# Performance work log

Measured on AMD Instinct MI355X. Metric: run time of the kernel, lower is better.

Reference implementation:

```python
import jax, jax.numpy as jnp
import numpy as np

B, D_IN, H, L, K, E, NL = 16384, 768, 1024, 128, 8192, 128, 3
CC = 0.25  # commitment cost
sg = jax.lax.stop_gradient


def _ln(x, g, b):
    # torch nn.LayerNorm, eps=1e-5
    m = jnp.mean(x, -1, keepdims=True)
    v = jnp.mean((x - m) ** 2, -1, keepdims=True)
    return (x - m) / jnp.sqrt(v + 1e-5) * g + b


def setup_inputs() -> dict:
    key = jax.random.key(0)
    ks = iter(jax.random.split(key, 32))
    def n(sh, s=0.02):
        return jax.random.normal(next(ks), sh, jnp.float32) * s
    return dict(
        x=jax.random.normal(next(ks), (B, D_IN), jnp.float32),
        eps=jax.random.normal(next(ks), (B, L), jnp.float32),
        enc_w1=n((D_IN, H)), enc_b1=jnp.zeros((H,), jnp.float32),
        enc_w2=n((H, H)), enc_b2=jnp.zeros((H,), jnp.float32),
        enc_w3=n((H, H)), enc_b3=jnp.zeros((H,), jnp.float32),
        mu_w=n((H, L)), mu_b=jnp.zeros((L,), jnp.float32),
        var_w=n((H, L)), var_b=jnp.zeros((L,), jnp.float32),
        dec_w1=n((L, H)), dec_b1=jnp.zeros((H,), jnp.float32),
        dec_w2=n((H, H)), dec_b2=jnp.zeros((H,), jnp.float32),
        dec_w3=n((H, D_IN)), dec_b3=jnp.zeros((D_IN,), jnp.float32),
        ln_g=jnp.ones((NL, L), jnp.float32),
        ln_b=jnp.zeros((NL, L), jnp.float32),
        q_in_w=n((NL, L, E)), q_in_b=jnp.zeros((NL, E), jnp.float32),
        codebook=jax.random.uniform(next(ks), (NL, K, E), jnp.float32,
                                    -1.0 / K, 1.0 / K),
        q_out_w=n((NL, E, L)), q_out_b=jnp.zeros((NL, L), jnp.float32),
    )


def reference(x, eps, enc_w1, enc_b1, enc_w2, enc_b2, enc_w3, enc_b3,
              mu_w, mu_b, var_w, var_b,
              dec_w1, dec_b1, dec_w2, dec_b2, dec_w3, dec_b3,
              ln_g, ln_b, q_in_w, q_in_b, codebook, q_out_w, q_out_b):
    # encoder MLP
    h = jax.nn.relu(x @ enc_w1 + enc_b1)
    h = jax.nn.relu(h @ enc_w2 + enc_b2)
    h = h @ enc_w3 + enc_b3
    mu = h @ mu_w + mu_b
    log_var = h @ var_w + var_b
    z = mu + eps * jnp.exp(0.5 * log_var)  # reparameterize

    # residual quantization over NL layers
    cur = z
    quantized = jnp.zeros_like(z)
    total_loss = jnp.float32(0.0)
    for i in range(NL):  # small fixed layer count
        nr = _ln(cur, ln_g[i], ln_b[i])                  # [B, L]
        f = nr @ q_in_w[i] + q_in_b[i]                   # [B, E]
        cb = codebook[i]                                 # [K, E]
        d = (jnp.sum(f * f, axis=1, keepdims=True)
             + jnp.sum(cb * cb, axis=1)
             - 2.0 * f @ cb.T)                           # [B, K]
        idx = jnp.argmin(d, axis=1)                      # [B]
        q = cb[idx] @ q_out_w[i] + q_out_b[i]            # gather == onehot@cb
        e_loss = jnp.mean((sg(q) - nr) ** 2)
        q_loss = jnp.mean((q - sg(nr)) ** 2)
        total_loss = total_loss + q_loss + CC * e_loss
        q_st = nr + sg(q - nr)                           # straight-through
        quantized = quantized + q_st
        cur = cur - q_st

    # decoder MLP
    r = jax.nn.relu(quantized @ dec_w1 + dec_b1)
    r = jax.nn.relu(r @ dec_w2 + dec_b2)
    recon = r @ dec_w3 + dec_b3
    return recon, mu, log_var, total_loss
```

## Files before the change

kernel.cpp:

```cpp
#include <hip/hip_runtime.h>
#include <stdint.h>


typedef float   floatx4  __attribute__((ext_vector_type(4)));
typedef __bf16  bf16x8   __attribute__((ext_vector_type(8)));
typedef unsigned short ushort4v __attribute__((ext_vector_type(4)));
typedef unsigned short bfbits;

#define AS1 __attribute__((address_space(1)))
#define AS3 __attribute__((address_space(3)))

__device__ __forceinline__ bfbits f2bf(float f) {
  unsigned u = __float_as_uint(f);
  u += 0x7fffu + ((u >> 16) & 1u);
  return (bfbits)(u >> 16);
}

__device__ __forceinline__ void load_lds16(const void* g, void* l) {
  __builtin_amdgcn_global_load_lds((AS1 void*)g, (AS3 void*)l, 16, 0, 0);
}

__global__ __launch_bounds__(256) void cvt_bf16_kernel(
    const float* __restrict__ in, bfbits* __restrict__ out, long n4) {
  long i = (long)blockIdx.x * 256 + threadIdx.x;
  if (i >= n4) return;
  float4 v = ((const float4*)in)[i];
  ushort4v o = { f2bf(v.x), f2bf(v.y), f2bf(v.z), f2bf(v.w) };
  ((ushort4v*)out)[i] = o;
}

__global__ __launch_bounds__(256) void transpose_bf16_kernel(
    const float* __restrict__ W, bfbits* __restrict__ Wt, int K, int N) {
  __shared__ float t[32][33];
  const long base = (long)blockIdx.z * K * N;
  const int k0 = blockIdx.y * 32, n0 = blockIdx.x * 32;
  const int tx = threadIdx.x & 31, ty = threadIdx.x >> 5;
#pragma unroll
  for (int j = 0; j < 32; j += 8)
    t[ty + j][tx] = W[base + (long)(k0 + ty + j) * N + n0 + tx];
  __syncthreads();
#pragma unroll
  for (int j = 0; j < 32; j += 8)
    Wt[base + (long)(n0 + ty + j) * K + k0 + tx] = f2bf(t[tx][ty + j]);
}

__global__ __launch_bounds__(256) void rownorm_kernel(
    const float* __restrict__ cb, float* __restrict__ out) {
  const int wave = threadIdx.x >> 6, lane = threadIdx.x & 63;
  const long row = (long)blockIdx.x * 4 + wave;
  const float* r = cb + row * 128;
  float a = r[lane], b = r[lane + 64];
  float s = a * a + b * b;
#pragma unroll
  for (int off = 1; off < 64; off <<= 1) s += __shfl_xor(s, off);
  if (lane == 0) out[row] = s;
}

template <bool RELU, bool OUTF32, bool DUAL>
__global__ __launch_bounds__(256) void gemm_kernel(
    const bfbits* __restrict__ A, const bfbits* __restrict__ Bt,
    const float* __restrict__ bias, bfbits* __restrict__ Cb,
    float* __restrict__ Cf, float* __restrict__ Cf2, int N, int Kd) {
  __shared__ bfbits Als[128 * 64];
  __shared__ bfbits Bls[128 * 64];
  const int tid = threadIdx.x;
  const int wave = tid >> 6, lane = tid & 63;
  const int wr = wave >> 1, wc = wave & 1;
  const int row0 = blockIdx.x << 7, col0 = blockIdx.y << 7;
  const int l15 = lane & 15, l16 = lane >> 4;
  const int jrow = lane >> 3;
  const int gchunk = (lane & 7) ^ jrow;

  floatx4 acc[4][4] = {};

  for (int k0 = 0; k0 < Kd; k0 += 64) {
    __syncthreads();
#pragma unroll
    for (int j = 0; j < 4; ++j) {
      const int gi = wave * 4 + j;
      const int r = gi * 8 + jrow;
      load_lds16(A + (long)(row0 + r) * Kd + (k0 + gchunk * 8),
                 Als + gi * 512 + lane * 8);
      load_lds16(Bt + (long)(col0 + r) * Kd + (k0 + gchunk * 8),
                 Bls + gi * 512 + lane * 8);
    }
    __syncthreads();
#pragma unroll
    for (int kk = 0; kk < 2; ++kk) {
      bf16x8 af[4], bf[4];
#pragma unroll
      for (int t = 0; t < 4; ++t) {
        const int ar = wr * 64 + t * 16 + l15;
        af[t] = *(const bf16x8*)(Als + ar * 64 + (((kk * 4 + l16) ^ (ar & 7)) * 8));
        const int br = wc * 64 + t * 16 + l15;
        bf[t] = *(const bf16x8*)(Bls + br * 64 + (((kk * 4 + l16) ^ (br & 7)) * 8));
      }
#pragma unroll
      for (int i = 0; i < 4; ++i)
#pragma unroll
        for (int jn = 0; jn < 4; ++jn)
          acc[i][jn] = __builtin_amdgcn_mfma_f32_16x16x32_bf16(
              af[i], bf[jn], acc[i][jn], 0, 0, 0);
    }
  }

#pragma unroll
  for (int mt = 0; mt < 4; ++mt) {
#pragma unroll
    for (int nt = 0; nt < 4; ++nt) {
      const int col = col0 + wc * 64 + nt * 16 + l15;
      const float bv = bias[col];
      const int rowb = row0 + wr * 64 + mt * 16 + l16 * 4;
#pragma unroll
      for (int r = 0; r < 4; ++r) {
        float v = acc[mt][nt][r] + bv;
        if (RELU) v = fmaxf(v, 0.f);
        if (DUAL) {
          if (col < 128) Cf[(long)(rowb + r) * 128 + col] = v;
          else           Cf2[(long)(rowb + r) * 128 + col - 128] = v;
        } else {
          const long idx = (long)(rowb + r) * N + col;
          if (OUTF32) Cf[idx] = v; else Cb[idx] = f2bf(v);
        }
      }
    }
  }
}

template <bool RELU, bool OUTF32>
__global__ __launch_bounds__(512, 2) void gemm256_kernel(
    const bfbits* __restrict__ A, const bfbits* __restrict__ Bt,
    const float* __restrict__ bias, bfbits* __restrict__ Cb,
    float* __restrict__ Cf, int N, int Kd) {
  __shared__ alignas(16) bfbits As[2][256 * 64];
  __shared__ alignas(16) bfbits Bs[2][256 * 64];
  const int tid = threadIdx.x;
  const int w = tid >> 6, lane = tid & 63;
  const int wr = w >> 2, wc = w & 3;
  const int l15 = lane & 15, l16 = lane >> 4;
  const int jrow = lane >> 3;
  const int gch = (lane & 7) ^ jrow;

  const int nbx = gridDim.x, nby = gridDim.y;
  const int nwg = nbx * nby;
  const int cpx = nwg >> 3;
  const int lid = blockIdx.y * nbx + blockIdx.x;
  const int swz = (lid & 7) * cpx + (lid >> 3);
  const int bm = swz / nby, bn = swz % nby;
  const long row0 = (long)bm << 8;
  const long col0 = (long)bn << 8;

  const int NT = Kd >> 6;

  auto stageA = [&](int t, int hh) {
    const bfbits* src = A + (row0 + hh * 128) * Kd + t * 64 + gch * 8;
    bfbits* dst = &As[t & 1][hh * 8192];
#pragma unroll
    for (int q = 0; q < 2; ++q) {
      const int gi = q * 8 + w;
      load_lds16(src + (long)(gi * 8 + jrow) * Kd, dst + gi * 512 + lane * 8);
    }
  };
  auto stageB = [&](int t, int hh) {
    const bfbits* src = Bt + (col0 + hh * 128) * Kd + t * 64 + gch * 8;
    bfbits* dst = &Bs[t & 1][hh * 8192];
#pragma unroll
    for (int q = 0; q < 2; ++q) {
      const int gi = q * 8 + w;
      load_lds16(src + (long)(gi * 8 + jrow) * Kd, dst + gi * 512 + lane * 8);
    }
  };

  auto rdA = [&](int p, int i, int kk) -> bf16x8 {
    const int r = wr * 128 + i * 16 + l15;
    return *(const bf16x8*)(&As[p][r * 64 + (((kk * 4 + l16) ^ (r & 7)) * 8)]);
  };
  auto rdB = [&](int p, int j, int kk) -> bf16x8 {
    const int r = wc * 64 + j * 16 + l15;
    return *(const bf16x8*)(&Bs[p][r * 64 + (((kk * 4 + l16) ^ (r & 7)) * 8)]);
  };

  floatx4 acc[8][4] = {};

  stageA(0, 0); stageA(0, 1); stageB(0, 0); stageB(0, 1);
  stageA(1, 0);
  asm volatile("s_waitcnt vmcnt(2)" ::: "memory");
  __builtin_amdgcn_s_barrier();

  for (int s = 0; s < NT; ++s) {
    const int p = s & 1;
    bf16x8 bfr[4];

    {
      bf16x8 af[4];
#pragma unroll
      for (int t = 0; t < 4; ++t) af[t] = rdA(p, t, 0);
#pragma unroll
      for (int t = 0; t < 4; ++t) bfr[t] = rdB(p, t, 0);
      if (s + 1 < NT) stageA(s + 1, 1);
      __builtin_amdgcn_s_barrier();
      asm volatile("s_waitcnt lgkmcnt(0)" ::: "memory");
      __builtin_amdgcn_sched_barrier(0);
      __builtin_amdgcn_s_setprio(1);
#pragma unroll
      for (int i = 0; i < 4; ++i)
#pragma unroll
        for (int j = 0; j < 4; ++j)
          acc[i][j] = __builtin_amdgcn_mfma_f32_16x16x32_bf16(
              af[i], bfr[j], acc[i][j], 0, 0, 0);
      __builtin_amdgcn_s_setprio(0);
      __builtin_amdgcn_s_barrier();
    }
    {
      bf16x8 af[4];
#pragma unroll
      for (int t = 0; t < 4; ++t) af[t] = rdA(p, 4 + t, 0);
      if (s + 1 < NT) stageB(s + 1, 0);
      __builtin_amdgcn_s_barrier();
      asm volatile("s_waitcnt lgkmcnt(0)" ::: "memory");
      __builtin_amdgcn_sched_barrier(0);
      __builtin_amdgcn_s_setprio(1);
#pragma unroll
      for (int i = 0; i < 4; ++i)
#pragma unroll
        for (int j = 0; j < 4; ++j)
          acc[4 + i][j] = __builtin_amdgcn_mfma_f32_16x16x32_bf16(
              af[i], bfr[j], acc[4 + i][j], 0, 0, 0);
      __builtin_amdgcn_s_setprio(0);
      __builtin_amdgcn_s_barrier();
    }
    {
      bf16x8 af[4];
#pragma unroll
      for (int t = 0; t < 4; ++t) af[t] = rdA(p, t, 1);
#pragma unroll
      for (int t = 0; t < 4; ++t) bfr[t] = rdB(p, t, 1);
      if (s + 1 < NT) stageB(s + 1, 1);
      __builtin_amdgcn_s_barrier();
      asm volatile("s_waitcnt lgkmcnt(0)" ::: "memory");
      __builtin_amdgcn_sched_barrier(0);
      __builtin_amdgcn_s_setprio(1);
#pragma unroll
      for (int i = 0; i < 4; ++i)
#pragma unroll
        for (int j = 0; j < 4; ++j)
          acc[i][j] = __builtin_amdgcn_mfma_f32_16x16x32_bf16(
              af[i], bfr[j], acc[i][j], 0, 0, 0);
      __builtin_amdgcn_s_setprio(0);
      __builtin_amdgcn_s_barrier();
    }
    {
      bf16x8 af[4];
#pragma unroll
      for (int t = 0; t < 4; ++t) af[t] = rdA(p, 4 + t, 1);
      __builtin_amdgcn_s_barrier();
      asm volatile("s_waitcnt lgkmcnt(0)" ::: "memory");
      __builtin_amdgcn_sched_barrier(0);
      __builtin_amdgcn_s_setprio(1);
#pragma unroll
      for (int i = 0; i < 4; ++i)
#pragma unroll
        for (int j = 0; j < 4; ++j)
          acc[4 + i][j] = __builtin_amdgcn_mfma_f32_16x16x32_bf16(
              af[i], bfr[j], acc[4 + i][j], 0, 0, 0);
      __builtin_amdgcn_s_setprio(0);
      __builtin_amdgcn_s_barrier();
    }
    if (s + 1 < NT) {
      if (s + 2 < NT) {
        stageA(s + 2, 0);
        asm volatile("s_waitcnt vmcnt(2)" ::: "memory");
      } else {
        asm volatile("s_waitcnt vmcnt(0)" ::: "memory");
      }
      __builtin_amdgcn_s_barrier();
    }
  }

#pragma unroll
  for (int i = 0; i < 8; ++i) {
    const long rowb = row0 + wr * 128 + i * 16 + l16 * 4;
#pragma unroll
    for (int j = 0; j < 4; ++j) {
      const int col = (int)col0 + wc * 64 + j * 16 + l15;
      const float bv = bias[col];
#pragma unroll
      for (int r = 0; r < 4; ++r) {
        float v = acc[i][j][r] + bv;
        if (RELU) v = fmaxf(v, 0.f);
        const long idx = (rowb + r) * N + col;
        if (OUTF32) Cf[idx] = v; else Cb[idx] = f2bf(v);
      }
    }
  }
}

template <bool OUTF32>
__global__ __launch_bounds__(256) void gemm_n128_kernel(
    const bfbits* __restrict__ A, const bfbits* __restrict__ Bt,
    const float* __restrict__ bias, bfbits* __restrict__ Cb,
    float* __restrict__ Cf) {
  __shared__ bfbits Als[64 * 64];
  __shared__ bfbits Bls[128 * 64];
  const int tid = threadIdx.x;
  const int wave = tid >> 6, lane = tid & 63;
  const int wr = wave >> 1, wc = wave & 1;
  const int row0 = blockIdx.x << 6;
  const int l15 = lane & 15, l16 = lane >> 4;
  const int jrow = lane >> 3;
  const int gchunk = (lane & 7) ^ jrow;

  floatx4 acc[2][4] = {};

  for (int k0 = 0; k0 < 128; k0 += 64) {
    __syncthreads();
    {
#pragma unroll
      for (int j = 0; j < 2; ++j) {
        const int gi = wave * 2 + j;
        const int r = gi * 8 + jrow;
        load_lds16(A + (long)(row0 + r) * 128 + (k0 + gchunk * 8),
                   Als + gi * 512 + lane * 8);
      }
#pragma unroll
      for (int j = 0; j < 4; ++j) {
        const int gi = wave * 4 + j;
        const int r = gi * 8 + jrow;
        load_lds16(Bt + (long)r * 128 + (k0 + gchunk * 8),
                   Bls + gi * 512 + lane * 8);
      }
    }
    __syncthreads();
#pragma unroll
    for (int kk = 0; kk < 2; ++kk) {
      bf16x8 af[2], bf[4];
#pragma unroll
      for (int t = 0; t < 2; ++t) {
        const int ar = wr * 32 + t * 16 + l15;
        af[t] = *(const bf16x8*)(Als + ar * 64 + (((kk * 4 + l16) ^ (ar & 7)) * 8));
      }
#pragma unroll
      for (int t = 0; t < 4; ++t) {
        const int br = wc * 64 + t * 16 + l15;
        bf[t] = *(const bf16x8*)(Bls + br * 64 + (((kk * 4 + l16) ^ (br & 7)) * 8));
      }
#pragma unroll
      for (int i = 0; i < 2; ++i)
#pragma unroll
        for (int jn = 0; jn < 4; ++jn)
          acc[i][jn] = __builtin_amdgcn_mfma_f32_16x16x32_bf16(
              af[i], bf[jn], acc[i][jn], 0, 0, 0);
    }
  }

#pragma unroll
  for (int mt = 0; mt < 2; ++mt) {
#pragma unroll
    for (int nt = 0; nt < 4; ++nt) {
      const int col = wc * 64 + nt * 16 + l15;
      const float bv = bias[col];
      const int rowb = row0 + wr * 32 + mt * 16 + l16 * 4;
#pragma unroll
      for (int r = 0; r < 4; ++r) {
        const float v = acc[mt][nt][r] + bv;
        const long idx = (long)(rowb + r) * 128 + col;
        if (OUTF32) Cf[idx] = v; else Cb[idx] = f2bf(v);
      }
    }
  }
}

__global__ __launch_bounds__(512, 2) void dist2_kernel(
    const bfbits* __restrict__ A,
    const bfbits* __restrict__ Bt,
    const float* __restrict__ cbnorm,
    int2* __restrict__ cand) {
  __shared__ alignas(16) bfbits Bls[2][128 * 128];
  const int tid = threadIdx.x;
  const int wave = tid >> 6, lane = tid & 63;
  const int wr = wave & 3, wc = wave >> 2;
  const int l15 = lane & 15, l16 = lane >> 4;
  const int row0 = blockIdx.y * 256;
  const int col0 = blockIdx.x * 2048;

  bf16x8 af[4][4];
#pragma unroll
  for (int mt = 0; mt < 4; ++mt)
#pragma unroll
    for (int s = 0; s < 4; ++s)
      af[mt][s] = *(const bf16x8*)(A + (long)(row0 + wr * 64 + mt * 16 + l15) * 128 +
                                   s * 32 + l16 * 8);

  auto stage = [&](int t, int p) {
    const bfbits* src = Bt + (long)(col0 + t * 128) * 128;
    bfbits* dst = &Bls[p][0];
#pragma unroll
    for (int q = 0; q < 4; ++q) {
      const int j = q * 512 + tid;
      const int c = j >> 4;
      const int g = (j & 15) ^ (c & 15);
      load_lds16(src + (long)c * 128 + g * 8, dst + (size_t)j * 8);
    }
  };

  stage(0, 0);

  float run_val[4][4];
  int   run_col[4][4];
#pragma unroll
  for (int mt = 0; mt < 4; ++mt)
#pragma unroll
    for (int r = 0; r < 4; ++r) { run_val[mt][r] = 3.0e38f; run_col[mt][r] = 0; }

  __syncthreads();

  for (int t = 0; t < 16; ++t) {
    const bfbits* buf = &Bls[t & 1][0];
    if (t + 1 < 16) stage(t + 1, (t + 1) & 1);

    float cn[4];
    int   colv[4];
#pragma unroll
    for (int nt = 0; nt < 4; ++nt) {
      const int cl = wc * 64 + nt * 16 + l15;
      cn[nt] = cbnorm[col0 + t * 128 + cl];
      colv[nt] = t * 128 + cl;
    }

    floatx4 acc[4][4] = {};
#pragma unroll
    for (int s = 0; s < 4; ++s) {
      bf16x8 bf[4];
#pragma unroll
      for (int nt = 0; nt < 4; ++nt) {
        const int cl = wc * 64 + nt * 16 + l15;
        bf[nt] = *(const bf16x8*)(buf + (size_t)cl * 128 +
                                  (size_t)(((s * 4 + l16) ^ l15)) * 8);
      }
#pragma unroll
      for (int mt = 0; mt < 4; ++mt)
#pragma unroll
        for (int nt = 0; nt < 4; ++nt)
          acc[mt][nt] = __builtin_amdgcn_mfma_f32_16x16x32_bf16(
              af[mt][s], bf[nt], acc[mt][nt], 0, 0, 0);
    }

#pragma unroll
    for (int mt = 0; mt < 4; ++mt)
#pragma unroll
      for (int nt = 0; nt < 4; ++nt)
#pragma unroll
        for (int r = 0; r < 4; ++r) {
          const float sc = fmaf(-2.0f, acc[mt][nt][r], cn[nt]);
          if (sc < run_val[mt][r]) { run_val[mt][r] = sc; run_col[mt][r] = colv[nt]; }
        }

    __syncthreads();
  }

#pragma unroll
  for (int mt = 0; mt < 4; ++mt)
#pragma unroll
    for (int r = 0; r < 4; ++r) {
      float v = run_val[mt][r];
      int   c = run_col[mt][r];
#pragma unroll
      for (int off = 1; off < 16; off <<= 1) {
        const float ov = __shfl_xor(v, off);
        const int   oc = __shfl_xor(c, off);
        if (ov < v || (ov == v && oc < c)) { v = ov; c = oc; }
      }
      if (l15 == 0) {
        const int row = row0 + wr * 64 + mt * 16 + l16 * 4 + r;
        cand[(long)row * 8 + blockIdx.x * 2 + wc] =
            make_int2(__float_as_int(v), col0 + c);
      }
    }
}

__global__ __launch_bounds__(256) void argmin8_kernel(
    const int2* __restrict__ cand, const float* __restrict__ cb,
    bfbits* __restrict__ cbg) {
  const int wave = threadIdx.x >> 6, lane = threadIdx.x & 63;
  const long row = (long)blockIdx.x * 4 + wave;
  float v = 3.0e38f; int k = 0x7fffffff;
  if (lane < 8) {
    int2 c = cand[row * 8 + lane];
    v = __int_as_float(c.x); k = c.y;
  }
#pragma unroll
  for (int off = 1; off < 8; off <<= 1) {
    float ov = __shfl_xor(v, off);
    int   ok = __shfl_xor(k, off);
    if (ov < v || (ov == v && ok < k)) { v = ov; k = ok; }
  }
  k = __shfl(k, 0);
  const float* src = cb + (long)k * 128;
  cbg[row * 128 + lane]      = f2bf(src[lane]);
  cbg[row * 128 + lane + 64] = f2bf(src[lane + 64]);
}

__device__ __forceinline__ void ln_row(float c0, float c1, int lane,
                                       const float* __restrict__ g,
                                       const float* __restrict__ bta,
                                       long row, bfbits* __restrict__ nrb,
                                       float* __restrict__ nrf) {
  float s = c0 + c1, sq = c0 * c0 + c1 * c1;
#pragma unroll
  for (int off = 1; off < 64; off <<= 1) {
    s += __shfl_xor(s, off);
    sq += __shfl_xor(sq, off);
  }
  const float m = s * (1.f / 128.f);
  const float var = fmaxf(sq * (1.f / 128.f) - m * m, 0.f);
  const float rstd = rsqrtf(var + 1e-5f);
  const float y0 = (c0 - m) * rstd * g[lane] + bta[lane];
  const float y1 = (c1 - m) * rstd * g[lane + 64] + bta[lane + 64];
  nrf[row * 128 + lane] = y0;
  nrf[row * 128 + lane + 64] = y1;
  nrb[row * 128 + lane] = f2bf(y0);
  nrb[row * 128 + lane + 64] = f2bf(y1);
}

__global__ __launch_bounds__(256) void reparam_ln_kernel(
    const float* __restrict__ mu, const float* __restrict__ lv,
    const float* __restrict__ eps, float* __restrict__ cur,
    float* __restrict__ qnt, const float* __restrict__ g,
    const float* __restrict__ bta, bfbits* __restrict__ nrb,
    float* __restrict__ nrf) {
  const int wave = threadIdx.x >> 6, lane = threadIdx.x & 63;
  const long row = (long)blockIdx.x * 4 + wave;
  const long i0 = row * 128 + lane, i1 = i0 + 64;
  const float z0 = mu[i0] + eps[i0] * expf(0.5f * lv[i0]);
  const float z1 = mu[i1] + eps[i1] * expf(0.5f * lv[i1]);
  cur[i0] = z0; cur[i1] = z1;
  qnt[i0] = 0.f; qnt[i1] = 0.f;
  ln_row(z0, z1, lane, g, bta, row, nrb, nrf);
}

template <bool DO_LN>
__global__ __launch_bounds__(256) void qupd_ln_kernel(
    const float* __restrict__ q, float* __restrict__ nrf,
    float* __restrict__ cur, float* __restrict__ qnt,
    const float* __restrict__ g, const float* __restrict__ bta,
    bfbits* __restrict__ nrb, float* __restrict__ lossp) {
  const int wave = threadIdx.x >> 6, lane = threadIdx.x & 63;
  const long row = (long)blockIdx.x * 4 + wave;
  const long i0 = row * 128 + lane, i1 = i0 + 64;
  const float q0 = q[i0], q1 = q[i1];
  const float d0 = q0 - nrf[i0], d1 = q1 - nrf[i1];
  qnt[i0] += q0; qnt[i1] += q1;
  float p = d0 * d0 + d1 * d1;
#pragma unroll
  for (int off = 1; off < 64; off <<= 1) p += __shfl_xor(p, off);
  __shared__ float sp[4];
  if (lane == 0) sp[wave] = p;
  __syncthreads();
  if (threadIdx.x == 0) lossp[blockIdx.x] = sp[0] + sp[1] + sp[2] + sp[3];
  if (DO_LN) {
    const float c0 = cur[i0] - q0, c1 = cur[i1] - q1;
    cur[i0] = c0; cur[i1] = c1;
    ln_row(c0, c1, lane, g, bta, row, nrb, nrf);
  }
}

__global__ __launch_bounds__(256) void loss_reduce_kernel(
    const float* __restrict__ lossp, float* __restrict__ out, int n) {
  float s = 0.f;
  for (int i = threadIdx.x; i < n; i += 256) s += lossp[i];
#pragma unroll
  for (int off = 1; off < 64; off <<= 1) s += __shfl_xor(s, off);
  __shared__ float sp[4];
  const int wave = threadIdx.x >> 6, lane = threadIdx.x & 63;
  if (lane == 0) sp[wave] = s;
  __syncthreads();
  if (threadIdx.x == 0)
    *out = (sp[0] + sp[1] + sp[2] + sp[3]) * (1.25f / 2097152.f);
}

static void launch_gemm(bool relu, bool outf32, const bfbits* A,
                        const bfbits* Bt, const float* bias, bfbits* Cb,
                        float* Cf, int M, int N, int Kd, hipStream_t s) {
  dim3 g(M / 128, N / 128), b(256);
  if (relu) {
    gemm_kernel<true, false, false><<<g, b, 0, s>>>(A, Bt, bias, Cb, Cf, nullptr, N, Kd);
  } else if (outf32) {
    gemm_kernel<false, true, false><<<g, b, 0, s>>>(A, Bt, bias, Cb, Cf, nullptr, N, Kd);
  } else {
    gemm_kernel<false, false, false><<<g, b, 0, s>>>(A, Bt, bias, Cb, Cf, nullptr, N, Kd);
  }
}

static void launch_gemm256(bool relu, bool outf32, const bfbits* A,
                           const bfbits* Bt, const float* bias, bfbits* Cb,
                           float* Cf, int M, int N, int Kd, hipStream_t s) {
  dim3 g(M / 256, N / 256), b(512);
  if (relu) {
    gemm256_kernel<true, false><<<g, b, 0, s>>>(A, Bt, bias, Cb, Cf, N, Kd);
  } else if (outf32) {
    gemm256_kernel<false, true><<<g, b, 0, s>>>(A, Bt, bias, Cb, Cf, N, Kd);
  } else {
    gemm256_kernel<false, false><<<g, b, 0, s>>>(A, Bt, bias, Cb, Cf, N, Kd);
  }
}

extern "C" void kernel_launch(void* const* d_in, const int* in_sizes, int n_in,
                              void* d_out, int out_size, void* d_ws,
                              size_t ws_size, hipStream_t stream) {
  (void)in_sizes; (void)n_in; (void)out_size; (void)ws_size;
  constexpr long B = 16384, DIN = 768, H = 1024, L = 128, K = 8192;

  const float* x    = (const float*)d_in[0];
  const float* eps  = (const float*)d_in[1];
  const float* ew1  = (const float*)d_in[2];
  const float* eb1  = (const float*)d_in[3];
  const float* ew2  = (const float*)d_in[4];
  const float* eb2  = (const float*)d_in[5];
  const float* ew3  = (const float*)d_in[6];
  const float* eb3  = (const float*)d_in[7];
  const float* muw  = (const float*)d_in[8];
  const float* mub  = (const float*)d_in[9];
  const float* vaw  = (const float*)d_in[10];
  const float* vab  = (const float*)d_in[11];
  const float* dw1  = (const float*)d_in[12];
  const float* db1  = (const float*)d_in[13];
  const float* dw2  = (const float*)d_in[14];
  const float* db2  = (const float*)d_in[15];
  const float* dw3  = (const float*)d_in[16];
  const float* db3  = (const float*)d_in[17];
  const float* lng  = (const float*)d_in[18];
  const float* lnb  = (const float*)d_in[19];
  const float* qinw = (const float*)d_in[20];
  const float* qinb = (const float*)d_in[21];
  const float* cb   = (const float*)d_in[22];
  const float* qow  = (const float*)d_in[23];
  const float* qob  = (const float*)d_in[24];

  float* out = (float*)d_out;
  float* out_mu   = out + B * DIN;
  float* out_lv   = out_mu + B * L;
  float* out_loss = out_lv + B * L;

  char* ws = (char*)d_ws;
  constexpr size_t O_W1T  = 0;
  constexpr size_t O_W2T  = O_W1T + 1024 * 768 * 2;
  constexpr size_t O_W3T  = O_W2T + 1024 * 1024 * 2;
  constexpr size_t O_MUT  = O_W3T + 1024 * 1024 * 2;
  constexpr size_t O_VART = O_MUT + 128 * 1024 * 2;
  constexpr size_t O_DW1T = O_VART + 128 * 1024 * 2;
  constexpr size_t O_DW2T = O_DW1T + 1024 * 128 * 2;
  constexpr size_t O_DW3T = O_DW2T + 1024 * 1024 * 2;
  constexpr size_t O_QINT = O_DW3T + 768 * 1024 * 2;
  constexpr size_t O_QOUT = O_QINT + 3 * 128 * 128 * 2;
  constexpr size_t O_CBB  = O_QOUT + 3 * 128 * 128 * 2;
  constexpr size_t O_CBN  = O_CBB + 3 * 8192 * 128 * 2;
  constexpr size_t O_B2   = O_CBN + 3 * 8192 * 4;
  constexpr size_t O_LOSSP= O_B2 + 256 * 4;
  constexpr size_t O_CUR  = O_LOSSP + 3 * 4096 * 4;
  constexpr size_t O_QNT  = O_CUR + B * L * 4;
  constexpr size_t O_NRF  = O_QNT + B * L * 4;
  constexpr size_t O_H1   = O_NRF + B * L * 4;
  constexpr size_t O_H2   = O_H1 + B * H * 2;
  constexpr size_t O_H3   = O_H2 + B * H * 2;
  constexpr size_t O_NRB  = O_H2;
  constexpr size_t O_FB   = O_H2 + B * L * 2;
  constexpr size_t O_CBG  = O_H2 + 2 * B * L * 2;
  constexpr size_t O_QBUF = O_H2 + 3 * B * L * 2;
  constexpr size_t O_CAND = O_H2 + 3 * B * L * 2 + B * L * 4;
  constexpr size_t O_XB   = O_H3;
  constexpr size_t O_QZB  = O_H3;

  bfbits* w1t  = (bfbits*)(ws + O_W1T);
  bfbits* w2t  = (bfbits*)(ws + O_W2T);
  bfbits* w3t  = (bfbits*)(ws + O_W3T);
  bfbits* mut  = (bfbits*)(ws + O_MUT);
  bfbits* vart = (bfbits*)(ws + O_VART);
  bfbits* dw1t = (bfbits*)(ws + O_DW1T);
  bfbits* dw2t = (bfbits*)(ws + O_DW2T);
  bfbits* dw3t = (bfbits*)(ws + O_DW3T);
  bfbits* qint = (bfbits*)(ws + O_QINT);
  bfbits* qout = (bfbits*)(ws + O_QOUT);
  bfbits* cbb  = (bfbits*)(ws + O_CBB);
  float*  cbn  = (float*)(ws + O_CBN);
  float*  bias2= (float*)(ws + O_B2);
  float*  lossp= (float*)(ws + O_LOSSP);
  float*  cur  = (float*)(ws + O_CUR);
  float*  qnt  = (float*)(ws + O_QNT);
  float*  nrf  = (float*)(ws + O_NRF);
  bfbits* h1   = (bfbits*)(ws + O_H1);
  bfbits* h2   = (bfbits*)(ws + O_H2);
  bfbits* h3   = (bfbits*)(ws + O_H3);
  bfbits* nrb  = (bfbits*)(ws + O_NRB);
  bfbits* fb   = (bfbits*)(ws + O_FB);
  bfbits* cbg  = (bfbits*)(ws + O_CBG);
  float*  qbuf = (float*)(ws + O_QBUF);
  int2*   cand = (int2*)(ws + O_CAND);
  bfbits* xb   = (bfbits*)(ws + O_XB);
  bfbits* qzb  = (bfbits*)(ws + O_QZB);
  bfbits* r1   = h1;
  bfbits* r2   = h2;

  cvt_bf16_kernel<<<dim3((B * DIN) / 4 / 256), dim3(256), 0, stream>>>(x, xb, (B * DIN) / 4);
  cvt_bf16_kernel<<<dim3((3 * K * 128) / 4 / 256), dim3(256), 0, stream>>>(cb, cbb, (3 * K * 128) / 4);
  transpose_bf16_kernel<<<dim3(1024 / 32, 768 / 32, 1), dim3(256), 0, stream>>>(ew1, w1t, 768, 1024);
  transpose_bf16_kernel<<<dim3(32, 32, 1), dim3(256), 0, stream>>>(ew2, w2t, 1024, 1024);
  transpose_bf16_kernel<<<dim3(32, 32, 1), dim3(256), 0, stream>>>(ew3, w3t, 1024, 1024);
  transpose_bf16_kernel<<<dim3(128 / 32, 32, 1), dim3(256), 0, stream>>>(muw, mut, 1024, 128);
  transpose_bf16_kernel<<<dim3(128 / 32, 32, 1), dim3(256), 0, stream>>>(vaw, vart, 1024, 128);
  transpose_bf16_kernel<<<dim3(32, 128 / 32, 1), dim3(256), 0, stream>>>(dw1, dw1t, 128, 1024);
  transpose_bf16_kernel<<<dim3(32, 32, 1), dim3(256), 0, stream>>>(dw2, dw2t, 1024, 1024);
  transpose_bf16_kernel<<<dim3(768 / 32, 32, 1), dim3(256), 0, stream>>>(dw3, dw3t, 1024, 768);
  transpose_bf16_kernel<<<dim3(4, 4, 3), dim3(256), 0, stream>>>(qinw, qint, 128, 128);
  transpose_bf16_kernel<<<dim3(4, 4, 3), dim3(256), 0, stream>>>(qow, qout, 128, 128);
  rownorm_kernel<<<dim3(3 * K / 4), dim3(256), 0, stream>>>(cb, cbn);
  hipMemcpyAsync(bias2, mub, 128 * 4, hipMemcpyDeviceToDevice, stream);
  hipMemcpyAsync(bias2 + 128, vab, 128 * 4, hipMemcpyDeviceToDevice, stream);

  launch_gemm256(true, false, xb, w1t, eb1, h1, nullptr, B, 1024, 768, stream);
  launch_gemm256(true, false, h1, w2t, eb2, h2, nullptr, B, 1024, 1024, stream);
  launch_gemm256(false, false, h2, w3t, eb3, h3, nullptr, B, 1024, 1024, stream);
  gemm_kernel<false, true, true><<<dim3(128, 2), dim3(256), 0, stream>>>(
      h3, mut, bias2, nullptr, out_mu, out_lv, 256, 1024);

  reparam_ln_kernel<<<dim3(B / 4), dim3(256), 0, stream>>>(
      out_mu, out_lv, eps, cur, qnt, lng, lnb, nrb, nrf);

  for (int i = 0; i < 3; ++i) {
    gemm_n128_kernel<false><<<dim3(B / 64), dim3(256), 0, stream>>>(
        nrb, qint + (size_t)i * 128 * 128, qinb + i * 128, fb, nullptr);
    dist2_kernel<<<dim3(4, 64), dim3(512), 0, stream>>>(
        fb, cbb + (size_t)i * K * 128, cbn + (size_t)i * K, cand);
    argmin8_kernel<<<dim3(B / 4), dim3(256), 0, stream>>>(
        cand, cb + (size_t)i * K * 128, cbg);
    gemm_n128_kernel<true><<<dim3(B / 64), dim3(256), 0, stream>>>(
        cbg, qout + (size_t)i * 128 * 128, qob + i * 128, nullptr, qbuf);
    if (i < 2) {
      qupd_ln_kernel<true><<<dim3(B / 4), dim3(256), 0, stream>>>(
          qbuf, nrf, cur, qnt, lng + (i + 1) * 128, lnb + (i + 1) * 128,
          nrb, lossp + (size_t)i * 4096);
    } else {
      qupd_ln_kernel<false><<<dim3(B / 4), dim3(256), 0, stream>>>(
          qbuf, nrf, cur, qnt, nullptr, nullptr, nullptr,
          lossp + (size_t)i * 4096);
    }
  }
  loss_reduce_kernel<<<dim3(1), dim3(256), 0, stream>>>(lossp, out_loss, 3 * 4096);

  cvt_bf16_kernel<<<dim3((B * L) / 4 / 256), dim3(256), 0, stream>>>(qnt, qzb, (B * L) / 4);
  launch_gemm(true, false, qzb, dw1t, db1, r1, nullptr, B, 1024, 128, stream);
  launch_gemm256(true, false, r1, dw2t, db2, r2, nullptr, B, 1024, 1024, stream);
  launch_gemm256(false, true, r2, dw3t, db3, nullptr, out, B, 768, 1024, stream);
}
```

Measured before the change: 663.2 us.

## Pack codebook index into score bits, reorder gemm256 B staging, swap final decoder gemm

The distance kernel now seeds the MFMA accumulator with -0.5*||c||^2 and takes a running max of f·c minus half the norm. The codebook index is packed into the low 13 mantissa bits of that score, so one fmaxf replaces a compare-and-select over value and index. This cuts VALU work and register pressure in the epilogue and halves candidate traffic, but truncating the mantissa can change argmin ties and near-ties. Separately, the gemm256 kernel issues both B-half stages earlier in one step, and the final decoder GEMM switches from the 256-tile kernel to the generic one.

```diff
diff --git a/kernel.cpp b/kernel.cpp
--- a/kernel.cpp
+++ b/kernel.cpp
@@ -215,7 +215,7 @@
       bf16x8 af[4];
 #pragma unroll
       for (int t = 0; t < 4; ++t) af[t] = rdA(p, 4 + t, 0);
-      if (s + 1 < NT) stageB(s + 1, 0);
+      if (s + 1 < NT) { stageB(s + 1, 0); stageB(s + 1, 1); }
       __builtin_amdgcn_s_barrier();
       asm volatile("s_waitcnt lgkmcnt(0)" ::: "memory");
       __builtin_amdgcn_sched_barrier(0);
@@ -235,7 +235,6 @@
       for (int t = 0; t < 4; ++t) af[t] = rdA(p, t, 1);
 #pragma unroll
       for (int t = 0; t < 4; ++t) bfr[t] = rdB(p, t, 1);
-      if (s + 1 < NT) stageB(s + 1, 1);
       __builtin_amdgcn_s_barrier();
       asm volatile("s_waitcnt lgkmcnt(0)" ::: "memory");
       __builtin_amdgcn_sched_barrier(0);
@@ -374,7 +373,7 @@
     const bfbits* __restrict__ A,
     const bfbits* __restrict__ Bt,
     const float* __restrict__ cbnorm,
-    int2* __restrict__ cand) {
+    float* __restrict__ cand) {
   __shared__ alignas(16) bfbits Bls[2][128 * 128];
   const int tid = threadIdx.x;
   const int wave = tid >> 6, lane = tid & 63;
@@ -406,11 +405,10 @@
   stage(0, 0);
 
   float run_val[4][4];
-  int   run_col[4][4];
 #pragma unroll
   for (int mt = 0; mt < 4; ++mt)
 #pragma unroll
-    for (int r = 0; r < 4; ++r) { run_val[mt][r] = 3.0e38f; run_col[mt][r] = 0; }
+    for (int r = 0; r < 4; ++r) run_val[mt][r] = -3.0e38f;
 
   __syncthreads();
 
@@ -418,18 +416,34 @@
     const bfbits* buf = &Bls[t & 1][0];
     if (t + 1 < 16) stage(t + 1, (t + 1) & 1);
 
-    float cn[4];
-    int   colv[4];
+    floatx4 initv[4];
+    int gcol[4];
 #pragma unroll
     for (int nt = 0; nt < 4; ++nt) {
       const int cl = wc * 64 + nt * 16 + l15;
-      cn[nt] = cbnorm[col0 + t * 128 + cl];
-      colv[nt] = t * 128 + cl;
-    }
-
-    floatx4 acc[4][4] = {};
-#pragma unroll
-    for (int s = 0; s < 4; ++s) {
+      const float half_cn = -0.5f * cbnorm[col0 + t * 128 + cl];
+      initv[nt] = (floatx4){half_cn, half_cn, half_cn, half_cn};
+      gcol[nt] = col0 + t * 128 + cl;
+    }
+
+    floatx4 acc[4][4];
+    {
+      bf16x8 bf[4];
+#pragma unroll
+      for (int nt = 0; nt < 4; ++nt) {
+        const int cl = wc * 64 + nt * 16 + l15;
+        bf[nt] = *(const bf16x8*)(buf + (size_t)cl * 128 +
+                                  (size_t)((l16 ^ l15)) * 8);
+      }
+#pragma unroll
+      for (int mt = 0; mt < 4; ++mt)
+#pragma unroll
+        for (int nt = 0; nt < 4; ++nt)
+          acc[mt][nt] = __builtin_amdgcn_mfma_f32_16x16x32_bf16(
+              af[mt][0], bf[nt], initv[nt], 0, 0, 0);
+    }
+#pragma unroll
+    for (int s = 1; s < 4; ++s) {
       bf16x8 bf[4];
 #pragma unroll
       for (int nt = 0; nt < 4; ++nt) {
@@ -451,8 +465,10 @@
       for (int nt = 0; nt < 4; ++nt)
 #pragma unroll
         for (int r = 0; r < 4; ++r) {
-          const float sc = fmaf(-2.0f, acc[mt][nt][r], cn[nt]);
-          if (sc < run_val[mt][r]) { run_val[mt][r] = sc; run_col[mt][r] = colv[nt]; }
+          const unsigned emb =
+              (__float_as_uint(acc[mt][nt][r]) & 0xFFFFE000u) |
+              (unsigned)gcol[nt];
+          run_val[mt][r] = fmaxf(run_val[mt][r], __uint_as_float(emb));
         }
 
     __syncthreads();
@@ -463,38 +479,28 @@
 #pragma unroll
     for (int r = 0; r < 4; ++r) {
       float v = run_val[mt][r];
-      int   c = run_col[mt][r];
-#pragma unroll
-      for (int off = 1; off < 16; off <<= 1) {
-        const float ov = __shfl_xor(v, off);
-        const int   oc = __shfl_xor(c, off);
-        if (ov < v || (ov == v && oc < c)) { v = ov; c = oc; }
-      }
+#pragma unroll
+      for (int off = 1; off < 16; off <<= 1)
+        v = fmaxf(v, __shfl_xor(v, off));
       if (l15 == 0) {
         const int row = row0 + wr * 64 + mt * 16 + l16 * 4 + r;
-        cand[(long)row * 8 + blockIdx.x * 2 + wc] =
-            make_int2(__float_as_int(v), col0 + c);
+        cand[(long)row * 8 + blockIdx.x * 2 + wc] = v;
       }
     }
 }
 
 __global__ __launch_bounds__(256) void argmin8_kernel(
-    const int2* __restrict__ cand, const float* __restrict__ cb,
+    const float* __restrict__ cand, const float* __restrict__ cb,
     bfbits* __restrict__ cbg) {
   const int wave = threadIdx.x >> 6, lane = threadIdx.x & 63;
   const long row = (long)blockIdx.x * 4 + wave;
-  float v = 3.0e38f; int k = 0x7fffffff;
-  if (lane < 8) {
-    int2 c = cand[row * 8 + lane];
-    v = __int_as_float(c.x); k = c.y;
-  }
-#pragma unroll
-  for (int off = 1; off < 8; off <<= 1) {
-    float ov = __shfl_xor(v, off);
-    int   ok = __shfl_xor(k, off);
-    if (ov < v || (ov == v && ok < k)) { v = ov; k = ok; }
-  }
-  k = __shfl(k, 0);
+  float v = -3.0e38f;
+  if (lane < 8) v = cand[row * 8 + lane];
+#pragma unroll
+  for (int off = 1; off < 8; off <<= 1)
+    v = fmaxf(v, __shfl_xor(v, off));
+  v = __shfl(v, 0);
+  const int k = (int)(__float_as_uint(v) & 0x1FFFu);
   const float* src = cb + (long)k * 128;
   cbg[row * 128 + lane]      = f2bf(src[lane]);
   cbg[row * 128 + lane + 64] = f2bf(src[lane + 64]);
@@ -694,7 +700,7 @@
   bfbits* fb   = (bfbits*)(ws + O_FB);
   bfbits* cbg  = (bfbits*)(ws + O_CBG);
   float*  qbuf = (float*)(ws + O_QBUF);
-  int2*   cand = (int2*)(ws + O_CAND);
+  float*  cand = (float*)(ws + O_CAND);
   bfbits* xb   = (bfbits*)(ws + O_XB);
   bfbits* qzb  = (bfbits*)(ws + O_QZB);
   bfbits* r1   = h1;
@@ -749,5 +755,5 @@
   cvt_bf16_kernel<<<dim3((B * L) / 4 / 256), dim3(256), 0, stream>>>(qnt, qzb, (B * L) / 4);
   launch_gemm(true, false, qzb, dw1t, db1, r1, nullptr, B, 1024, 128, stream);
   launch_gemm256(true, false, r1, dw2t, db2, r2, nullptr, B, 1024, 1024, stream);
-  launch_gemm256(false, true, r2, dw3t, db3, nullptr, out, B, 768, 1024, stream);
-}
+  launch_gemm(false, true, r2, dw3t, db3, nullptr, out, B, 768, 1024, stream);
+}
```

Result: faster. 638.8 us (-3.7%).
